# Kernel tuning notes

Hardware: AMD Instinct MI355X
Metric: run time of the kernel (lower is better)

Reference implementation:

```python
import jax, jax.numpy as jnp
import numpy as np

S, B, E = 2048, 2, 768
H = 12
D = E // H  # 64
SCALE = D ** -0.5


def setup_inputs() -> dict:
    key = jax.random.key(0)
    ks = jax.random.split(key, 10)
    inp = {
        "query": jax.random.normal(ks[0], (S, B, E), dtype=jnp.float32),
        "attn_bias": jax.random.normal(ks[1], (B * H, S, S), dtype=jnp.float32) * 0.1,
        "key_padding_mask": jax.random.randint(ks[2], (B, S), 0, 2).astype(bool),
        "Wq": jax.random.normal(ks[3], (E, E), dtype=jnp.float32) * (E ** -0.5),
        "bq": jnp.zeros((E,), dtype=jnp.float32),
        "Wk": jax.random.normal(ks[4], (E, E), dtype=jnp.float32) * (E ** -0.5),
        "bk": jnp.zeros((E,), dtype=jnp.float32),
        "Wv": jax.random.normal(ks[5], (E, E), dtype=jnp.float32) * (E ** -0.5),
        "bv": jnp.zeros((E,), dtype=jnp.float32),
        "Wo": jax.random.normal(ks[6], (E, E), dtype=jnp.float32) * (E ** -0.5),
        "bo": jnp.zeros((E,), dtype=jnp.float32),
    }
    return inp


def reference(query, attn_bias, key_padding_mask, Wq, bq, Wk, bk, Wv, bv, Wo, bo):
    s, b, e = query.shape
    # projections (torch Linear: x @ W.T + b)
    q = (query @ Wq.T + bq) * SCALE
    k = query @ Wk.T + bk
    v = query @ Wv.T + bv
    # [s, b, e] -> [b*h, s, d]
    def to_heads(x):
        return x.reshape(s, b * H, D).transpose(1, 0, 2)
    q, k, v = to_heads(q), to_heads(k), to_heads(v)
    # scores [b*h, s_q, s_k]
    scores = jnp.einsum('nqd,nkd->nqk', q, k) + attn_bias
    # key padding mask: [b, s_k] -> broadcast over heads and queries
    scores = scores.reshape(b, H, s, s)
    scores = jnp.where(key_padding_mask[:, None, None, :], -jnp.inf, scores)
    scores = scores.reshape(b * H, s, s)
    probs = jax.nn.softmax(scores, axis=-1)
    attn = jnp.einsum('nqk,nkd->nqd', probs, v)  # [b*h, s, d]
    attn = attn.transpose(1, 0, 2).reshape(s, b, e)
    return attn @ Wo.T + bo
```

## Files before the change

### kernel.cpp

```cpp
#include <hip/hip_runtime.h>
#include <hip/hip_bf16.h>

typedef __attribute__((ext_vector_type(8))) short s16x8;
typedef __attribute__((ext_vector_type(4))) float f32x4;
typedef unsigned short u16;
typedef unsigned int u32;

#define SDIM 2048
#define BDIM 2
#define HDIM 12
#define DDIM 64
#define EDIM 768
#define MDIM 4096
#define SCALE_Q 0.125f
#define KSPLIT 1024
#define NIT (KSPLIT / 32)
#define HFRAG 131072

static __device__ __forceinline__ f32x4 zero4() {
    f32x4 v; v[0] = v[1] = v[2] = v[3] = 0.f; return v;
}

static __device__ __forceinline__ u16 f2b(float x) {
    u32 u = __builtin_bit_cast(u32, x);
    u32 lsb = (u >> 16) & 1u;
    u += 0x7fffu + lsb;
    return (u16)(u >> 16);
}

static __device__ __forceinline__ f32x4 mfma16(s16x8 a, s16x8 b, f32x4 c) {
    return __builtin_amdgcn_mfma_f32_16x16x32_bf16(a, b, c, 0, 0, 0);
}

static __device__ __forceinline__ void gload_lds16(const void* g, void* l) {
    __builtin_amdgcn_global_load_lds(
        (const __attribute__((address_space(1))) void*)g,
        (__attribute__((address_space(3))) void*)l, 16, 0, 0);
}

__global__ void mask_bits_kernel(const u32* __restrict__ raw, u32* __restrict__ outbits) {
    __shared__ int okInt, okFloat;
    int t = threadIdx.x;
    if (t == 0) { okInt = 1; okFloat = 1; }
    __syncthreads();
    int li = 1, lf = 1;
    for (int i = t; i < 1024; i += blockDim.x) {
        u32 v = raw[i];
        if (v > 1u) li = 0;
        if (v != 0u && v != 0x3F800000u) lf = 0;
    }
    if (!li) atomicAnd(&okInt, 0);
    if (!lf) atomicAnd(&okFloat, 0);
    __syncthreads();
    const unsigned char* rb = (const unsigned char*)raw;
    if (t < (BDIM * SDIM) / 32) {
        u32 bits = 0;
        for (int j = 0; j < 32; ++j) {
            int i = t * 32 + j;
            int v;
            if (okInt)        v = (int)raw[i];
            else if (okFloat) v = (raw[i] != 0u) ? 1 : 0;
            else              v = (int)rb[i];
            bits |= (v ? 1u : 0u) << j;
        }
        outbits[t] = bits;
    }
}

__global__ __launch_bounds__(256) void conv_f32_bf16(
    const float* __restrict__ s, u16* __restrict__ d, int n8)
{
    int i = blockIdx.x * 256 + threadIdx.x;
    if (i >= n8) return;
    float4 x0 = ((const float4*)s)[(size_t)i * 2];
    float4 x1 = ((const float4*)s)[(size_t)i * 2 + 1];
    uint4 o;
    o.x = (u32)f2b(x0.x) | ((u32)f2b(x0.y) << 16);
    o.y = (u32)f2b(x0.z) | ((u32)f2b(x0.w) << 16);
    o.z = (u32)f2b(x1.x) | ((u32)f2b(x1.y) << 16);
    o.w = (u32)f2b(x1.z) | ((u32)f2b(x1.w) << 16);
    ((uint4*)d)[i] = o;
}

__global__ __launch_bounds__(256) void gemm_xwT(
    const u16* __restrict__ A, const u16* __restrict__ Wb,
    const float* __restrict__ bias, float scale,
    u16* __restrict__ out_sc, float* __restrict__ out_rm, int mode)
{
    __shared__ u16 Al[64 * 56];
    __shared__ u16 Bl[64 * 56];
    int tid = threadIdx.x;
    int mb = blockIdx.x * 64, nb = blockIdx.y * 64;
    int lane = tid & 63, w = tid >> 6;
    int r16 = lane & 15, g4 = lane >> 4;
    int wm = w >> 1, wn = w & 1;

    f32x4 acc[2][2];
    acc[0][0] = zero4(); acc[0][1] = zero4(); acc[1][0] = zero4(); acc[1][1] = zero4();

    int srow = tid >> 2, scol = (tid & 3) * 8;

    for (int kb = 0; kb < EDIM; kb += 32) {
        __syncthreads();
        *(uint4*)&Al[srow * 56 + scol] =
            *(const uint4*)&A[(size_t)(mb + srow) * EDIM + kb + scol];
        *(uint4*)&Bl[srow * 56 + scol] =
            *(const uint4*)&Wb[(size_t)(nb + srow) * EDIM + kb + scol];
        __syncthreads();
        s16x8 a[2], bb[2];
        #pragma unroll
        for (int mi = 0; mi < 2; ++mi)
            a[mi] = *(const s16x8*)&Al[(wm * 32 + mi * 16 + r16) * 56 + g4 * 8];
        #pragma unroll
        for (int ni = 0; ni < 2; ++ni)
            bb[ni] = *(const s16x8*)&Bl[(wn * 32 + ni * 16 + r16) * 56 + g4 * 8];
        #pragma unroll
        for (int mi = 0; mi < 2; ++mi)
            #pragma unroll
            for (int ni = 0; ni < 2; ++ni)
                acc[mi][ni] = mfma16(a[mi], bb[ni], acc[mi][ni]);
    }

    #pragma unroll
    for (int mi = 0; mi < 2; ++mi) {
        #pragma unroll
        for (int ni = 0; ni < 2; ++ni) {
            int n = nb + wn * 32 + ni * 16 + r16;
            float bv = bias[n];
            #pragma unroll
            for (int r = 0; r < 4; ++r) {
                int m = mb + wm * 32 + mi * 16 + g4 * 4 + r;
                float c = (acc[mi][ni][r] + bv) * scale;
                if (mode == 1) {
                    int s_ = m >> 1, b_ = m & 1, h_ = n >> 6, d_ = n & 63;
                    out_sc[((size_t)(b_ * HDIM + h_) * SDIM + s_) * DDIM + d_] = f2b(c);
                } else if (mode == 3) {
                    int s_ = m >> 1, b_ = m & 1, h_ = n >> 6, d_ = n & 63;
                    size_t p = (size_t)(b_ * HDIM + h_) * HFRAG
                             + (size_t)(s_ >> 4) * 1024 + (size_t)((d_ >> 5) & 1) * 512
                             + (size_t)(((d_ >> 3) & 3) * 16 + (s_ & 15)) * 8 + (d_ & 7);
                    out_sc[p] = f2b(c);
                } else if (mode == 4) {
                    int s_ = m >> 1, b_ = m & 1, h_ = n >> 6, d_ = n & 63;
                    size_t p = (size_t)(b_ * HDIM + h_) * HFRAG
                             + (size_t)(s_ >> 5) * 2048 + (size_t)((d_ >> 4) & 3) * 512
                             + (size_t)(((s_ >> 3) & 3) * 16 + (d_ & 15)) * 8 + (s_ & 7);
                    out_sc[p] = f2b(c);
                } else {
                    out_rm[(size_t)m * EDIM + n] = c;
                }
            }
        }
    }
}

struct KV { s16x8 k0, k1, k2, k3, v0, v1, v2, v3; };

__global__ __launch_bounds__(128) void attn_fused(
    const u16* __restrict__ qw, const u16* __restrict__ kf_g,
    const u16* __restrict__ vf_g, const float* __restrict__ bias,
    const u32* __restrict__ maskBits, u16* __restrict__ attn_out)
{
    __shared__ __align__(1024) unsigned char SM[21504];

    int flat = blockIdx.y * 64 + blockIdx.x;
    int virt = (flat & 7) * 192 + (flat >> 3);
    int qt = virt & 63, bh = virt >> 6;

    int tid = threadIdx.x;
    int w = tid >> 6, lane = tid & 63;
    int r16 = lane & 15, g4 = lane >> 4;
    int qbase = qt * 32;
    int b_ = bh / HDIM, h_ = bh % HDIM;
    const u16* Q  = qw   + (size_t)bh * SDIM * DDIM;
    const u16* KF = kf_g + (size_t)bh * HFRAG;
    const u16* VF = vf_g + (size_t)bh * HFRAG;
    const float* BrowQ = bias + (size_t)bh * SDIM * SDIM + (size_t)qbase * SDIM;
    const u32* mB = maskBits + b_ * (SDIM / 32);

    unsigned char* wb = SM + w * 10752;
    float* RingW = (float*)wb;
    u16*   Pl    = (u16*)(wb + 8192);

    s16x8 qf[2][2];
    #pragma unroll
    for (int h = 0; h < 2; ++h) {
        qf[h][0] = *(const s16x8*)&Q[(size_t)(qbase + 16 * h + r16) * DDIM + g4 * 8];
        qf[h][1] = *(const s16x8*)&Q[(size_t)(qbase + 16 * h + r16) * DDIM + g4 * 8 + 32];
    }

    f32x4 accO[2][4];
    #pragma unroll
    for (int h = 0; h < 2; ++h)
        #pragma unroll
        for (int dt = 0; dt < 4; ++dt) accO[h][dt] = zero4();
    float m_run[2] = {-1e30f, -1e30f}, l_run[2] = {0.f, 0.f};

    const int k0 = w * KSPLIT;

    auto issue_kv = [&](int t, KV& dst) {
        int tc = t < NIT ? t : NIT - 1;
        int kbn = k0 + tc * 32;
        const u16* KT = KF + (size_t)(kbn >> 4) * 1024;
        dst.k0 = *(const s16x8*)&KT[lane * 8];
        dst.k1 = *(const s16x8*)&KT[512 + lane * 8];
        dst.k2 = *(const s16x8*)&KT[1024 + lane * 8];
        dst.k3 = *(const s16x8*)&KT[1536 + lane * 8];
        const u16* VT = VF + (size_t)(kbn >> 5) * 2048;
        dst.v0 = *(const s16x8*)&VT[lane * 8];
        dst.v1 = *(const s16x8*)&VT[512 + lane * 8];
        dst.v2 = *(const s16x8*)&VT[1024 + lane * 8];
        dst.v3 = *(const s16x8*)&VT[1536 + lane * 8];
    };

    auto stage_bias = [&](int t) {
        int tc = t < NIT ? t : NIT - 1;
        int kb = k0 + tc * 32;
        unsigned char* slot = (unsigned char*)(RingW + (t & 1) * 1024);
        int sq = (lane & 7) ^ ((lane >> 3) & 7);
        #pragma unroll
        for (int j = 0; j < 4; ++j) {
            int row = j * 8 + (lane >> 3);
            gload_lds16(&BrowQ[(size_t)row * SDIM + kb + sq * 4], slot + j * 1024);
        }
    };

    auto compute = [&](int t, KV& cur) {
        u32 mw = mB[__builtin_amdgcn_readfirstlane((k0 + t * 32) >> 5)];
        const float* Bs = RingW + (t & 1) * 1024;
        f32x4 sc[2][2];
        #pragma unroll
        for (int h = 0; h < 2; ++h) {
            sc[h][0] = mfma16(cur.k1, qf[h][1], mfma16(cur.k0, qf[h][0], zero4()));
            sc[h][1] = mfma16(cur.k3, qf[h][1], mfma16(cur.k2, qf[h][0], zero4()));
        }
        #pragma unroll
        for (int h = 0; h < 2; ++h) {
            int rr = 16 * h + r16;
            #pragma unroll
            for (int kt = 0; kt < 2; ++kt) {
                float4 bc = *(const float4*)&Bs[rr * 32 + (((4 * kt + g4) ^ (r16 & 7)) * 4)];
                u32 mseg = (mw >> (16 * kt + 4 * g4)) & 0xF;
                sc[h][kt][0] = (mseg & 1) ? -1e30f : sc[h][kt][0] + bc.x;
                sc[h][kt][1] = (mseg & 2) ? -1e30f : sc[h][kt][1] + bc.y;
                sc[h][kt][2] = (mseg & 4) ? -1e30f : sc[h][kt][2] + bc.z;
                sc[h][kt][3] = (mseg & 8) ? -1e30f : sc[h][kt][3] + bc.w;
            }
        }
        #pragma unroll
        for (int h = 0; h < 2; ++h) {
            float pm = fmaxf(
                fmaxf(fmaxf(sc[h][0][0], sc[h][0][1]), fmaxf(sc[h][0][2], sc[h][0][3])),
                fmaxf(fmaxf(sc[h][1][0], sc[h][1][1]), fmaxf(sc[h][1][2], sc[h][1][3])));
            pm = fmaxf(pm, __shfl_xor(pm, 16));
            pm = fmaxf(pm, __shfl_xor(pm, 32));
            bool norescale = __all(pm <= m_run[h] + 4.f);
            float mn = norescale ? m_run[h] : fmaxf(m_run[h], pm);
            float p[8];
            #pragma unroll
            for (int kt = 0; kt < 2; ++kt)
                #pragma unroll
                for (int r = 0; r < 4; ++r)
                    p[kt * 4 + r] = __expf(sc[h][kt][r] - mn);
            float ps = ((p[0] + p[1]) + (p[2] + p[3])) + ((p[4] + p[5]) + (p[6] + p[7]));
            ps += __shfl_xor(ps, 16);
            ps += __shfl_xor(ps, 32);
            if (norescale) {
                l_run[h] += ps;
            } else {
                float alpha = __expf(m_run[h] - mn);
                l_run[h] = l_run[h] * alpha + ps;
                m_run[h] = mn;
                float aR0 = __shfl(alpha, g4 * 4 + 0);
                float aR1 = __shfl(alpha, g4 * 4 + 1);
                float aR2 = __shfl(alpha, g4 * 4 + 2);
                float aR3 = __shfl(alpha, g4 * 4 + 3);
                #pragma unroll
                for (int dt = 0; dt < 4; ++dt) {
                    accO[h][dt][0] *= aR0;
                    accO[h][dt][1] *= aR1;
                    accO[h][dt][2] *= aR2;
                    accO[h][dt][3] *= aR3;
                }
            }
            int rr = 16 * h + r16;
            #pragma unroll
            for (int kt = 0; kt < 2; ++kt) {
                uint2 pv;
                pv.x = (u32)f2b(p[kt * 4 + 0]) | ((u32)f2b(p[kt * 4 + 1]) << 16);
                pv.y = (u32)f2b(p[kt * 4 + 2]) | ((u32)f2b(p[kt * 4 + 3]) << 16);
                *(uint2*)&Pl[rr * 40 + kt * 16 + g4 * 4] = pv;
            }
        }
        #pragma unroll
        for (int h = 0; h < 2; ++h) {
            s16x8 pf = *(const s16x8*)&Pl[(16 * h + r16) * 40 + g4 * 8];
            accO[h][0] = mfma16(pf, cur.v0, accO[h][0]);
            accO[h][1] = mfma16(pf, cur.v1, accO[h][1]);
            accO[h][2] = mfma16(pf, cur.v2, accO[h][2]);
            accO[h][3] = mfma16(pf, cur.v3, accO[h][3]);
        }
    };

    KV A, B;
    issue_kv(0, A);
    stage_bias(0);

    for (int t = 0; t < NIT; t += 2) {
        issue_kv(t + 1, B);
        stage_bias(t + 1);
        asm volatile("s_waitcnt vmcnt(12)" ::: "memory");
        __builtin_amdgcn_sched_barrier(0);
        compute(t, A);

        issue_kv(t + 2, A);
        stage_bias(t + 2);
        asm volatile("s_waitcnt vmcnt(12)" ::: "memory");
        __builtin_amdgcn_sched_barrier(0);
        compute(t + 1, B);
    }

    __syncthreads();
    float* As = (float*)SM;
    float* Ml = (float*)(SM + 17408);
    float* Ll = Ml + 64;
    #pragma unroll
    for (int h = 0; h < 2; ++h)
        #pragma unroll
        for (int dt = 0; dt < 4; ++dt)
            #pragma unroll
            for (int r = 0; r < 4; ++r)
                As[(size_t)(w * 32 + 16 * h + g4 * 4 + r) * 68 + dt * 16 + r16] = accO[h][dt][r];
    if (g4 == 0) {
        #pragma unroll
        for (int h = 0; h < 2; ++h) {
            Ml[w * 32 + 16 * h + r16] = m_run[h];
            Ll[w * 32 + 16 * h + r16] = l_run[h];
        }
    }
    __syncthreads();

    #pragma unroll
    for (int h = 0; h < 2; ++h) {
        #pragma unroll
        for (int dg = 0; dg < 2; ++dg) {
            int d = w * 32 + dg * 16 + r16;
            #pragma unroll
            for (int r = 0; r < 4; ++r) {
                int q = 16 * h + g4 * 4 + r;
                float m0 = Ml[q], m1 = Ml[32 + q];
                float mt = fmaxf(m0, m1);
                float e0 = __expf(m0 - mt), e1 = __expf(m1 - mt);
                float lt = Ll[q] * e0 + Ll[32 + q] * e1;
                float o = (As[(size_t)q * 68 + d] * e0 + As[(size_t)(32 + q) * 68 + d] * e1) / lt;
                attn_out[((size_t)(qbase + q) * BDIM + b_) * EDIM + h_ * DDIM + d] = f2b(o);
            }
        }
    }
}

extern "C" void kernel_launch(void* const* d_in, const int* in_sizes, int n_in,
                              void* d_out, int out_size, void* d_ws, size_t ws_size,
                              hipStream_t stream) {
    const float* query     = (const float*)d_in[0];
    const float* attn_bias = (const float*)d_in[1];
    const u32*   mask_raw  = (const u32*)d_in[2];
    const float* Wq = (const float*)d_in[3];
    const float* bq = (const float*)d_in[4];
    const float* Wk = (const float*)d_in[5];
    const float* bk = (const float*)d_in[6];
    const float* Wv = (const float*)d_in[7];
    const float* bv = (const float*)d_in[8];
    const float* Wo = (const float*)d_in[9];
    const float* bo = (const float*)d_in[10];
    float* out = (float*)d_out;

    char* ws = (char*)d_ws;
    u32* maskB = (u32*)ws;
    const size_t HEADSZ = (size_t)BDIM * HDIM * SDIM * DDIM;
    const size_t WSZ = (size_t)EDIM * EDIM;
    u16* qws = (u16*)(ws + 16384);
    u16* kws = qws + HEADSZ;
    u16* vws = kws + HEADSZ;
    u16* aws = vws + HEADSZ;
    u16* qbf = aws;
    u16* wWq = aws + HEADSZ;
    u16* wWk = wWq + WSZ;
    u16* wWv = wWk + WSZ;
    u16* wWo = wWv + WSZ;

    mask_bits_kernel<<<1, 256, 0, stream>>>(mask_raw, maskB);

    conv_f32_bf16<<<(int)(MDIM * EDIM / 8 / 256), 256, 0, stream>>>(query, qbf, MDIM * EDIM / 8);
    conv_f32_bf16<<<(int)(WSZ / 8 / 256), 256, 0, stream>>>(Wq, wWq, (int)(WSZ / 8));
    conv_f32_bf16<<<(int)(WSZ / 8 / 256), 256, 0, stream>>>(Wk, wWk, (int)(WSZ / 8));
    conv_f32_bf16<<<(int)(WSZ / 8 / 256), 256, 0, stream>>>(Wv, wWv, (int)(WSZ / 8));
    conv_f32_bf16<<<(int)(WSZ / 8 / 256), 256, 0, stream>>>(Wo, wWo, (int)(WSZ / 8));

    dim3 gg(MDIM / 64, EDIM / 64);
    gemm_xwT<<<gg, 256, 0, stream>>>(qbf, wWq, bq, SCALE_Q, qws, nullptr, 1);
    gemm_xwT<<<gg, 256, 0, stream>>>(qbf, wWk, bk, 1.0f,    kws, nullptr, 3);
    gemm_xwT<<<gg, 256, 0, stream>>>(qbf, wWv, bv, 1.0f,    vws, nullptr, 4);

    dim3 ga(64, BDIM * HDIM);
    attn_fused<<<ga, 128, 0, stream>>>(qws, kws, vws, attn_bias, maskB, aws);

    gemm_xwT<<<gg, 256, 0, stream>>>(aws, wWo, bo, 1.0f, nullptr, out, 0);
}
```

Before: 233.3 us.

## Enlarge GEMM tiles to 128x128 with direct-to-LDS loads; deepen attention bias ring

The projection GEMM now uses 128x128 output tiles with a 4x4 MFMA grid per wave, and stages A/W tiles with global-to-LDS direct loads in a k-chunk-major layout instead of register round-trips. This raises operand reuse per LDS fetch and cuts global traffic, at the cost of fewer blocks (192 per GEMM) and more accumulator registers. Separately, the attention kernel's per-wave bias ring grows from 2 to 4 slots with a prefetch distance of 3 tiles to hide latency on the large fp32 bias stream. That uses more shared memory per block, which may reduce occupancy.

```diff
diff --git a/kernel.cpp b/kernel.cpp
--- a/kernel.cpp
+++ b/kernel.cpp
@@ -87,49 +87,55 @@
     const float* __restrict__ bias, float scale,
     u16* __restrict__ out_sc, float* __restrict__ out_rm, int mode)
 {
-    __shared__ u16 Al[64 * 56];
-    __shared__ u16 Bl[64 * 56];
+    __shared__ u16 Al[4096];
+    __shared__ u16 Bl[4096];
     int tid = threadIdx.x;
-    int mb = blockIdx.x * 64, nb = blockIdx.y * 64;
+    int mb = blockIdx.x * 128, nb = blockIdx.y * 128;
     int lane = tid & 63, w = tid >> 6;
     int r16 = lane & 15, g4 = lane >> 4;
     int wm = w >> 1, wn = w & 1;
 
-    f32x4 acc[2][2];
-    acc[0][0] = zero4(); acc[0][1] = zero4(); acc[1][0] = zero4(); acc[1][1] = zero4();
-
-    int srow = tid >> 2, scol = (tid & 3) * 8;
+    f32x4 acc[4][4];
+    #pragma unroll
+    for (int mi = 0; mi < 4; ++mi)
+        #pragma unroll
+        for (int ni = 0; ni < 4; ++ni) acc[mi][ni] = zero4();
 
     for (int kb = 0; kb < EDIM; kb += 32) {
         __syncthreads();
-        *(uint4*)&Al[srow * 56 + scol] =
-            *(const uint4*)&A[(size_t)(mb + srow) * EDIM + kb + scol];
-        *(uint4*)&Bl[srow * 56 + scol] =
-            *(const uint4*)&Wb[(size_t)(nb + srow) * EDIM + kb + scol];
+        #pragma unroll
+        for (int j = 0; j < 2; ++j) {
+            gload_lds16(&A[(size_t)(mb + j * 64 + lane) * EDIM + kb + w * 8],
+                        (char*)Al + (w * 2 + j) * 1024);
+            gload_lds16(&Wb[(size_t)(nb + j * 64 + lane) * EDIM + kb + w * 8],
+                        (char*)Bl + (w * 2 + j) * 1024);
+        }
+        asm volatile("s_waitcnt vmcnt(0)" ::: "memory");
         __syncthreads();
-        s16x8 a[2], bb[2];
-        #pragma unroll
-        for (int mi = 0; mi < 2; ++mi)
-            a[mi] = *(const s16x8*)&Al[(wm * 32 + mi * 16 + r16) * 56 + g4 * 8];
-        #pragma unroll
-        for (int ni = 0; ni < 2; ++ni)
-            bb[ni] = *(const s16x8*)&Bl[(wn * 32 + ni * 16 + r16) * 56 + g4 * 8];
-        #pragma unroll
-        for (int mi = 0; mi < 2; ++mi)
-            #pragma unroll
-            for (int ni = 0; ni < 2; ++ni)
-                acc[mi][ni] = mfma16(a[mi], bb[ni], acc[mi][ni]);
-    }
-
-    #pragma unroll
-    for (int mi = 0; mi < 2; ++mi) {
-        #pragma unroll
-        for (int ni = 0; ni < 2; ++ni) {
-            int n = nb + wn * 32 + ni * 16 + r16;
+
+        s16x8 a[4], b[4];
+        #pragma unroll
+        for (int mi = 0; mi < 4; ++mi)
+            a[mi] = *(const s16x8*)&Al[g4 * 1024 + (wm * 64 + mi * 16 + r16) * 8];
+        #pragma unroll
+        for (int ni = 0; ni < 4; ++ni)
+            b[ni] = *(const s16x8*)&Bl[g4 * 1024 + (wn * 64 + ni * 16 + r16) * 8];
+        #pragma unroll
+        for (int mi = 0; mi < 4; ++mi)
+            #pragma unroll
+            for (int ni = 0; ni < 4; ++ni)
+                acc[mi][ni] = mfma16(a[mi], b[ni], acc[mi][ni]);
+    }
+
+    #pragma unroll
+    for (int mi = 0; mi < 4; ++mi) {
+        #pragma unroll
+        for (int ni = 0; ni < 4; ++ni) {
+            int n = nb + wn * 64 + ni * 16 + r16;
             float bv = bias[n];
             #pragma unroll
             for (int r = 0; r < 4; ++r) {
-                int m = mb + wm * 32 + mi * 16 + g4 * 4 + r;
+                int m = mb + wm * 64 + mi * 16 + g4 * 4 + r;
                 float c = (acc[mi][ni][r] + bv) * scale;
                 if (mode == 1) {
                     int s_ = m >> 1, b_ = m & 1, h_ = n >> 6, d_ = n & 63;
@@ -161,7 +167,7 @@
     const u16* __restrict__ vf_g, const float* __restrict__ bias,
     const u32* __restrict__ maskBits, u16* __restrict__ attn_out)
 {
-    __shared__ __align__(1024) unsigned char SM[21504];
+    __shared__ __align__(1024) unsigned char SM[37888];
 
     int flat = blockIdx.y * 64 + blockIdx.x;
     int virt = (flat & 7) * 192 + (flat >> 3);
@@ -178,9 +184,9 @@
     const float* BrowQ = bias + (size_t)bh * SDIM * SDIM + (size_t)qbase * SDIM;
     const u32* mB = maskBits + b_ * (SDIM / 32);
 
-    unsigned char* wb = SM + w * 10752;
+    unsigned char* wb = SM + w * 18944;
     float* RingW = (float*)wb;
-    u16*   Pl    = (u16*)(wb + 8192);
+    u16*   Pl    = (u16*)(wb + 16384);
 
     s16x8 qf[2][2];
     #pragma unroll
@@ -216,7 +222,7 @@
     auto stage_bias = [&](int t) {
         int tc = t < NIT ? t : NIT - 1;
         int kb = k0 + tc * 32;
-        unsigned char* slot = (unsigned char*)(RingW + (t & 1) * 1024);
+        unsigned char* slot = wb + (tc & 3) * 4096;
         int sq = (lane & 7) ^ ((lane >> 3) & 7);
         #pragma unroll
         for (int j = 0; j < 4; ++j) {
@@ -227,7 +233,7 @@
 
     auto compute = [&](int t, KV& cur) {
         u32 mw = mB[__builtin_amdgcn_readfirstlane((k0 + t * 32) >> 5)];
-        const float* Bs = RingW + (t & 1) * 1024;
+        const float* Bs = RingW + (t & 3) * 1024;
         f32x4 sc[2][2];
         #pragma unroll
         for (int h = 0; h < 2; ++h) {
@@ -305,17 +311,19 @@
     KV A, B;
     issue_kv(0, A);
     stage_bias(0);
+    stage_bias(1);
+    stage_bias(2);
 
     for (int t = 0; t < NIT; t += 2) {
         issue_kv(t + 1, B);
-        stage_bias(t + 1);
-        asm volatile("s_waitcnt vmcnt(12)" ::: "memory");
+        stage_bias(t + 3);
+        asm volatile("s_waitcnt vmcnt(16)" ::: "memory");
         __builtin_amdgcn_sched_barrier(0);
         compute(t, A);
 
         issue_kv(t + 2, A);
-        stage_bias(t + 2);
-        asm volatile("s_waitcnt vmcnt(12)" ::: "memory");
+        stage_bias(t + 4);
+        asm volatile("s_waitcnt vmcnt(16)" ::: "memory");
         __builtin_amdgcn_sched_barrier(0);
         compute(t + 1, B);
     }
@@ -397,7 +405,7 @@
     conv_f32_bf16<<<(int)(WSZ / 8 / 256), 256, 0, stream>>>(Wv, wWv, (int)(WSZ / 8));
     conv_f32_bf16<<<(int)(WSZ / 8 / 256), 256, 0, stream>>>(Wo, wWo, (int)(WSZ / 8));
 
-    dim3 gg(MDIM / 64, EDIM / 64);
+    dim3 gg(MDIM / 128, EDIM / 128);
     gemm_xwT<<<gg, 256, 0, stream>>>(qbf, wWq, bq, SCALE_Q, qws, nullptr, 1);
     gemm_xwT<<<gg, 256, 0, stream>>>(qbf, wWk, bk, 1.0f,    kws, nullptr, 3);
     gemm_xwT<<<gg, 256, 0, stream>>>(qbf, wWv, bv, 1.0f,    vws, nullptr, 4);
```

After: 296.7 us. 27.2% more time.
